# Kernel tuning notes

Measured on AMD Instinct MI355X. Metric: run time of the kernel, lower is better.

The kernel has to match this reference:

```python
import jax, jax.numpy as jnp
import numpy as np

ATTN_BLOCK_SIZE = 1024
NUM_BUCKETS = 32  # int(sqrt(1024))


def _bucket_index():
    # Static index matching the torch init:
    # arange2 = ((arange1 - indices) % S) // num_buckets, then pick columns arange(nb)*nb
    S, nb = ATTN_BLOCK_SIZE, NUM_BUCKETS
    ar = np.arange(S)
    a2 = ((ar[:, None] - ar[None, :]) % S) // nb          # (S, S), values in [0, nb)
    a2 = a2[:, np.arange(nb) * nb]                         # (S, nb)
    return jnp.asarray(a2, dtype=jnp.int32)


def _decay_sum(x, alpha, beta, past_steps):
    # result[t] = alpha * sum_{i=0}^{P-1} beta**i * x[t-1-i]  (zeros for t-1-i < 0)
    # == the torch pad-and-add loop, expressed as one causal depthwise conv.
    B, S, D = x.shape
    P = past_steps
    w = alpha * beta ** jnp.arange(P, dtype=x.dtype)       # (P,) decay weights
    k = jnp.broadcast_to(w[::-1][None, None, :], (D, 1, P))  # depthwise kernel (O=D, I/g=1, W=P)
    xc = jnp.transpose(x, (0, 2, 1))                       # (B, D, S)
    y = jax.lax.conv_general_dilated(
        xc, k, window_strides=(1,), padding=[(P, 0)],
        dimension_numbers=('NCW', 'OIW', 'NCW'), feature_group_count=D,
    )[..., :S]                                             # (B, D, S)
    return jnp.transpose(y, (0, 2, 1))                     # (B, S, D)


def setup_inputs() -> dict:
    key = jax.random.key(0)
    k1, k2, k3, k4, k5 = jax.random.split(key, 5)
    B, S, nb = 1024, ATTN_BLOCK_SIZE, NUM_BUCKETS
    return {
        "x": jax.random.normal(k1, (B, S, nb), dtype=jnp.float32),
        "alpha": jax.random.uniform(k2, (1,), dtype=jnp.float32),
        "beta": jax.random.uniform(k3, (1,), dtype=jnp.float32),
        "pos_fwd_param": jax.random.normal(k4, (1, nb), dtype=jnp.float32),
        "pos_bwd_param": jax.random.normal(k5, (1, nb), dtype=jnp.float32),
        "past_steps": 128,
    }


def reference(x, alpha, beta, pos_fwd_param, pos_bwd_param, past_steps):
    S = ATTN_BLOCK_SIZE
    result = _decay_sum(x, alpha, beta, past_steps)        # (B, S, nb)
    ones = jnp.ones((S, 1), dtype=x.dtype)
    pb_fwd = ones @ pos_fwd_param                          # (S, nb)
    pb_bwd = jnp.take_along_axis(ones @ pos_bwd_param, _bucket_index(), axis=-1)  # (S, nb)
    return result + pb_fwd + pb_bwd
```

## Files before the change

kernel.cpp:

```cpp
#include <hip/hip_runtime.h>


typedef float f32x4 __attribute__((ext_vector_type(4)));

constexpr int S    = 1024;
constexpr int D    = 32;
constexpr int CL   = 16;
constexpr int NCH  = S / CL;
constexpr int LAG  = 8;
constexpr int KEEP = 8;
constexpr int NTHR = NCH * (D / 4);

__global__ __launch_bounds__(NTHR, 8)
void attn_pred_kernel(const float* __restrict__ x,
                      const float* __restrict__ alpha_p,
                      const float* __restrict__ beta_p,
                      const float* __restrict__ pos_fwd,
                      const float* __restrict__ pos_bwd,
                      const int*   __restrict__ past_p,
                      float* __restrict__ out)
{
    __shared__ f32x4 sA[NCH][D / 4];
    __shared__ f32x4 sC[NCH][D / 4];

    const int tid  = threadIdx.x;
    const int b    = blockIdx.x;
    const int lane = tid & 63;
    const int wv   = tid >> 6;
    const int g    = lane >> 3;
    const int dg   = lane & 7;
    const int c    = g * 8 + wv;
    const int s0   = c * CL;

    const float alpha = alpha_p[0];
    const float beta  = beta_p[0];
    const int   P     = past_p[0];

    double bb = (double)beta, bpd = 1.0;
    for (int e = P; e; e >>= 1) { if (e & 1) bpd *= bb; bb *= bb; }
    const float bP = (float)bpd;
    double b16 = (double)beta;
    for (int i = 0; i < 4; ++i) b16 *= b16;
    const float bCL = (float)b16;
    const float aP  = alpha * bP;
    const float m   = (g > 0) ? -aP : 0.f;

    const int d0 = dg * 4;
    const int q  = c >> 1;
    const f32x4 pf = reinterpret_cast<const f32x4*>(pos_fwd)[dg];
    f32x4 add;
    add.x = pf.x + pos_bwd[(q - (d0 + 0)) & (D - 1)];
    add.y = pf.y + pos_bwd[(q - (d0 + 1)) & (D - 1)];
    add.z = pf.z + pos_bwd[(q - (d0 + 2)) & (D - 1)];
    add.w = pf.w + pos_bwd[(q - (d0 + 3)) & (D - 1)];

    const f32x4* xg = reinterpret_cast<const f32x4*>(x) + (size_t)b * S * (D / 4) + dg;

    f32x4 xr[KEEP];
    #pragma unroll
    for (int i = 0; i < KEEP; ++i)
        xr[i] = xg[(s0 + i) * (D / 4)];

    f32x4 A = {0.f, 0.f, 0.f, 0.f};
    #pragma unroll
    for (int i = 0; i < KEEP; ++i) {
        A.x = fmaf(beta, A.x, xr[i].x);
        A.y = fmaf(beta, A.y, xr[i].y);
        A.z = fmaf(beta, A.z, xr[i].z);
        A.w = fmaf(beta, A.w, xr[i].w);
    }
    #pragma unroll
    for (int i = KEEP; i < CL; ++i) {
        const f32x4 v = xg[(s0 + i) * (D / 4)];
        A.x = fmaf(beta, A.x, v.x);
        A.y = fmaf(beta, A.y, v.y);
        A.z = fmaf(beta, A.z, v.z);
        A.w = fmaf(beta, A.w, v.w);
    }
    sA[c][dg] = A;
    __syncthreads();

    if (tid < D / 4) {
        f32x4 run = {0.f, 0.f, 0.f, 0.f};
        for (int cc = 0; cc < NCH; ++cc) {
            sC[cc][tid] = run;
            const f32x4 Ac = sA[cc][tid];
            f32x4 z;
            if (cc >= LAG) {
                const f32x4 Al = sA[cc - LAG][tid];
                z.x = alpha * fmaf(-bP, Al.x, Ac.x);
                z.y = alpha * fmaf(-bP, Al.y, Ac.y);
                z.z = alpha * fmaf(-bP, Al.z, Ac.z);
                z.w = alpha * fmaf(-bP, Al.w, Ac.w);
            } else {
                z.x = alpha * Ac.x; z.y = alpha * Ac.y;
                z.z = alpha * Ac.z; z.w = alpha * Ac.w;
            }
            run.x = fmaf(bCL, run.x, z.x);
            run.y = fmaf(bCL, run.y, z.y);
            run.z = fmaf(bCL, run.z, z.z);
            run.w = fmaf(bCL, run.w, z.w);
        }
    }
    __syncthreads();
    f32x4 y = sC[c][dg];

    f32x4* og = reinterpret_cast<f32x4*>(out) + ((size_t)b * S + s0) * (D / 4) + dg;
    #pragma unroll
    for (int i = 0; i < KEEP; ++i) {
        f32x4 o;
        o.x = y.x + add.x; o.y = y.y + add.y;
        o.z = y.z + add.z; o.w = y.w + add.w;
        __builtin_nontemporal_store(o, &og[i * (D / 4)]);

        f32x4 xl;
        xl.x = __shfl_up(xr[i].x, 8);
        xl.y = __shfl_up(xr[i].y, 8);
        xl.z = __shfl_up(xr[i].z, 8);
        xl.w = __shfl_up(xr[i].w, 8);

        y.x = fmaf(beta, y.x, fmaf(alpha, xr[i].x, m * xl.x));
        y.y = fmaf(beta, y.y, fmaf(alpha, xr[i].y, m * xl.y));
        y.z = fmaf(beta, y.z, fmaf(alpha, xr[i].z, m * xl.z));
        y.w = fmaf(beta, y.w, fmaf(alpha, xr[i].w, m * xl.w));
    }
    #pragma unroll
    for (int i = KEEP; i < CL; ++i) {
        const f32x4 xt = xg[(s0 + i) * (D / 4)];

        f32x4 o;
        o.x = y.x + add.x; o.y = y.y + add.y;
        o.z = y.z + add.z; o.w = y.w + add.w;
        __builtin_nontemporal_store(o, &og[i * (D / 4)]);

        f32x4 xl;
        xl.x = __shfl_up(xt.x, 8);
        xl.y = __shfl_up(xt.y, 8);
        xl.z = __shfl_up(xt.z, 8);
        xl.w = __shfl_up(xt.w, 8);

        y.x = fmaf(beta, y.x, fmaf(alpha, xt.x, m * xl.x));
        y.y = fmaf(beta, y.y, fmaf(alpha, xt.y, m * xl.y));
        y.z = fmaf(beta, y.z, fmaf(alpha, xt.z, m * xl.z));
        y.w = fmaf(beta, y.w, fmaf(alpha, xt.w, m * xl.w));
    }
}

extern "C" void kernel_launch(void* const* d_in, const int* in_sizes, int n_in,
                              void* d_out, int out_size, void* d_ws, size_t ws_size,
                              hipStream_t stream) {
    const float* x  = (const float*)d_in[0];
    const float* al = (const float*)d_in[1];
    const float* be = (const float*)d_in[2];
    const float* pf = (const float*)d_in[3];
    const float* pb = (const float*)d_in[4];
    const int*   ps = (const int*)d_in[5];
    float* out = (float*)d_out;

    const int B = in_sizes[0] / (S * D);
    attn_pred_kernel<<<dim3(B), NTHR, 0, stream>>>(x, al, be, pf, pb, ps, out);
}
```

Measured before the change: 244.7 us.

## Replace serial chunk scan with parallel 8-chunk windowed lookback

Removes the single-wave serial scan over 64 chunk summaries and the second barrier. Each thread now computes its chunk's starting state directly by combining the previous LAG chunk summaries with powers of beta^16, which holds because contributions older than the window cancel. It also XOR-swizzles the shared-memory layout to avoid bank conflicts, prefetches four rows before the barrier, drops the register-kept first half of x, and switches to regular stores instead of nontemporal stores. The cost is eight LDS reads per thread and more global reloads of x in place of register reuse.

```diff
diff --git a/kernel.cpp b/kernel.cpp
--- a/kernel.cpp
+++ b/kernel.cpp
@@ -8,7 +8,6 @@
 constexpr int CL   = 16;
 constexpr int NCH  = S / CL;
 constexpr int LAG  = 8;
-constexpr int KEEP = 8;
 constexpr int NTHR = NCH * (D / 4);
 
 __global__ __launch_bounds__(NTHR, 8)
@@ -21,7 +20,6 @@
                       float* __restrict__ out)
 {
     __shared__ f32x4 sA[NCH][D / 4];
-    __shared__ f32x4 sC[NCH][D / 4];
 
     const int tid  = threadIdx.x;
     const int b    = blockIdx.x;
@@ -56,82 +54,51 @@
 
     const f32x4* xg = reinterpret_cast<const f32x4*>(x) + (size_t)b * S * (D / 4) + dg;
 
-    f32x4 xr[KEEP];
-    #pragma unroll
-    for (int i = 0; i < KEEP; ++i)
-        xr[i] = xg[(s0 + i) * (D / 4)];
-
     f32x4 A = {0.f, 0.f, 0.f, 0.f};
     #pragma unroll
-    for (int i = 0; i < KEEP; ++i) {
-        A.x = fmaf(beta, A.x, xr[i].x);
-        A.y = fmaf(beta, A.y, xr[i].y);
-        A.z = fmaf(beta, A.z, xr[i].z);
-        A.w = fmaf(beta, A.w, xr[i].w);
-    }
-    #pragma unroll
-    for (int i = KEEP; i < CL; ++i) {
+    for (int i = 0; i < CL; ++i) {
         const f32x4 v = xg[(s0 + i) * (D / 4)];
         A.x = fmaf(beta, A.x, v.x);
         A.y = fmaf(beta, A.y, v.y);
         A.z = fmaf(beta, A.z, v.z);
         A.w = fmaf(beta, A.w, v.w);
     }
-    sA[c][dg] = A;
-    __syncthreads();
+    sA[c][dg ^ (g & 7)] = A;
 
-    if (tid < D / 4) {
-        f32x4 run = {0.f, 0.f, 0.f, 0.f};
-        for (int cc = 0; cc < NCH; ++cc) {
-            sC[cc][tid] = run;
-            const f32x4 Ac = sA[cc][tid];
-            f32x4 z;
-            if (cc >= LAG) {
-                const f32x4 Al = sA[cc - LAG][tid];
-                z.x = alpha * fmaf(-bP, Al.x, Ac.x);
-                z.y = alpha * fmaf(-bP, Al.y, Ac.y);
-                z.z = alpha * fmaf(-bP, Al.z, Ac.z);
-                z.w = alpha * fmaf(-bP, Al.w, Ac.w);
-            } else {
-                z.x = alpha * Ac.x; z.y = alpha * Ac.y;
-                z.z = alpha * Ac.z; z.w = alpha * Ac.w;
-            }
-            run.x = fmaf(bCL, run.x, z.x);
-            run.y = fmaf(bCL, run.y, z.y);
-            run.z = fmaf(bCL, run.z, z.z);
-            run.w = fmaf(bCL, run.w, z.w);
-        }
+    f32x4 p0 = xg[(s0 + 0) * (D / 4)];
+    f32x4 p1 = xg[(s0 + 1) * (D / 4)];
+    f32x4 p2 = xg[(s0 + 2) * (D / 4)];
+    f32x4 p3 = xg[(s0 + 3) * (D / 4)];
+
+    asm volatile("s_waitcnt lgkmcnt(0)" ::: "memory");
+    __builtin_amdgcn_s_barrier();
+    __builtin_amdgcn_sched_barrier(0);
+
+    f32x4 h = {0.f, 0.f, 0.f, 0.f};
+    #pragma unroll
+    for (int k = LAG; k >= 1; --k) {
+        const int idx = c - k;
+        f32x4 Ak = {0.f, 0.f, 0.f, 0.f};
+        if (idx >= 0) Ak = sA[idx][dg ^ ((idx >> 3) & 7)];
+        h.x = fmaf(bCL, h.x, Ak.x);
+        h.y = fmaf(bCL, h.y, Ak.y);
+        h.z = fmaf(bCL, h.z, Ak.z);
+        h.w = fmaf(bCL, h.w, Ak.w);
     }
-    __syncthreads();
-    f32x4 y = sC[c][dg];
+    f32x4 y;
+    y.x = alpha * h.x; y.y = alpha * h.y;
+    y.z = alpha * h.z; y.w = alpha * h.w;
 
     f32x4* og = reinterpret_cast<f32x4*>(out) + ((size_t)b * S + s0) * (D / 4) + dg;
     #pragma unroll
-    for (int i = 0; i < KEEP; ++i) {
-        f32x4 o;
-        o.x = y.x + add.x; o.y = y.y + add.y;
-        o.z = y.z + add.z; o.w = y.w + add.w;
-        __builtin_nontemporal_store(o, &og[i * (D / 4)]);
-
-        f32x4 xl;
-        xl.x = __shfl_up(xr[i].x, 8);
-        xl.y = __shfl_up(xr[i].y, 8);
-        xl.z = __shfl_up(xr[i].z, 8);
-        xl.w = __shfl_up(xr[i].w, 8);
-
-        y.x = fmaf(beta, y.x, fmaf(alpha, xr[i].x, m * xl.x));
-        y.y = fmaf(beta, y.y, fmaf(alpha, xr[i].y, m * xl.y));
-        y.z = fmaf(beta, y.z, fmaf(alpha, xr[i].z, m * xl.z));
-        y.w = fmaf(beta, y.w, fmaf(alpha, xr[i].w, m * xl.w));
-    }
-    #pragma unroll
-    for (int i = KEEP; i < CL; ++i) {
-        const f32x4 xt = xg[(s0 + i) * (D / 4)];
+    for (int i = 0; i < CL; ++i) {
+        const f32x4 xt = (i == 0) ? p0 : (i == 1) ? p1 : (i == 2) ? p2 : (i == 3) ? p3
+                                   : xg[(s0 + i) * (D / 4)];
 
         f32x4 o;
         o.x = y.x + add.x; o.y = y.y + add.y;
         o.z = y.z + add.z; o.w = y.w + add.w;
-        __builtin_nontemporal_store(o, &og[i * (D / 4)]);
+        og[i * (D / 4)] = o;
 
         f32x4 xl;
         xl.x = __shfl_up(xt.x, 8);
```

After: 260.2 us. 6.3% more time.
